# Kernel optimization log

Hardware: AMD Instinct MI355X
Metric: run time of the kernel (lower is better)

The kernel has to match this reference:

```python
import jax, jax.numpy as jnp
import numpy as np

# ---- static config (matches init_kwargs and NSA hyperparams in source) ----
DIM = 512; HEADS = 8; DH = DIM // HEADS; DEPTH = 2
HH = 28; WW = 28; SEQ = HH * WW            # 784
WIN = 28 * 7                                # sliding window = 196
CBS = 28 * 14; CST = 28 * 7                 # compress block 392, stride 196
SBS = 28 * 14; NSEL = 1                     # selection block 392, top-1
NC = (SEQ - CBS) // CST + 1                 # 3 compressed blocks
NS = SEQ // SBS                             # 2 selection blocks
EPS = 1e-5
BATCH = 8


def _overlap_matrix():
    # fraction of each compressed block overlapping each selection block
    O = np.zeros((NC, NS), np.float32)
    for i in range(NC):
        a, b = i * CST, i * CST + CBS
        for j in range(NS):
            c, d = j * SBS, (j + 1) * SBS
            O[i, j] = max(0, min(b, d) - max(a, c)) / CBS
    return jnp.asarray(O)

OVERLAP = _overlap_matrix()  # [NC, NS]


def setup_inputs() -> dict:
    key = jax.random.key(0)
    ks = jax.random.split(key, 12)
    p = lambda i, shape, s=0.02: (jax.random.normal(ks[i], shape, jnp.float32) * s)
    return {
        "x": jax.random.normal(ks[0], (BATCH, DIM, HH, WW), jnp.float32),
        "pos_emb": jax.random.normal(ks[1], (SEQ,), jnp.float32),
        "attn_norm_g": jnp.ones((DEPTH, DIM), jnp.float32),
        "Wq": p(2, (DEPTH, DIM, HEADS * DH)),
        "Wk": p(3, (DEPTH, DIM, HEADS * DH)),
        "Wv": p(4, (DEPTH, DIM, HEADS * DH)),
        "Wo": p(5, (DEPTH, HEADS * DH, DIM)),
        "Wg": p(6, (DEPTH, DIM, HEADS * 3)),
        "ff_norm_g": jnp.ones((DEPTH, DIM), jnp.float32),
        "ff_norm_b": jnp.zeros((DEPTH, DIM), jnp.float32),
        "ff_w1": p(7, (DEPTH, 4 * DIM, DIM)),
        "ff_b1": jnp.zeros((DEPTH, 4 * DIM), jnp.float32),
        "ff_w2": p(8, (DEPTH, DIM, 4 * DIM)),
        "ff_b2": jnp.zeros((DEPTH, DIM), jnp.float32),
    }


def _sparse_attn(x, g, wq, wk, wv, wo, wg):
    # x: [b, n, d]  -- NSA: sliding window + compressed + top-k block selection
    b, n, d = x.shape
    xr = x * jax.lax.rsqrt(jnp.mean(x * x, -1, keepdims=True) + EPS) * g  # RMSNorm
    q = (xr @ wq).reshape(b, n, HEADS, DH)
    k = (xr @ wk).reshape(b, n, HEADS, DH)
    v = (xr @ wv).reshape(b, n, HEADS, DH)
    scale = DH ** -0.5

    # ---- compressed branch: mean-pool overlapping blocks ----
    ck = jnp.stack([k[:, i * CST:i * CST + CBS].mean(1) for i in range(NC)], 1)  # [b,NC,h,dh]
    cv = jnp.stack([v[:, i * CST:i * CST + CBS].mean(1) for i in range(NC)], 1)
    sc = jnp.einsum('bihd,bjhd->bhij', q, ck) * scale          # [b,h,n,NC]
    pc = jax.nn.softmax(sc, -1)
    out_c = jnp.einsum('bhij,bjhd->bihd', pc, cv)              # [b,n,h,dh]

    # ---- selection branch: importance -> top-k selection blocks -> fine attn ----
    imp = jnp.einsum('bhij,jk->bhik', pc, OVERLAP)             # [b,h,n,NS]
    _, sel = jax.lax.top_k(imp, NSEL)                          # [b,h,n,NSEL]
    selmask = jax.nn.one_hot(sel, NS, dtype=jnp.float32).sum(-2) > 0  # [b,h,n,NS]
    blk = jnp.arange(n) // SBS                                 # token -> selection block
    tokmask = selmask[..., blk]                                # [b,h,n,n]
    sf = jnp.einsum('bihd,bjhd->bhij', q, k) * scale           # full fine scores (shared)
    neg = jnp.finfo(sf.dtype).min
    ps = jax.nn.softmax(jnp.where(tokmask, sf, neg), -1)
    out_s = jnp.einsum('bhij,bjhd->bihd', ps, v)

    # ---- sliding window branch ----
    idx = jnp.arange(n)
    winmask = jnp.abs(idx[:, None] - idx[None, :]) < WIN       # [n,n]
    pw = jax.nn.softmax(jnp.where(winmask, sf, neg), -1)
    out_w = jnp.einsum('bhij,bjhd->bihd', pw, v)

    # ---- per-head learned gates over the 3 branches ----
    gates = jax.nn.sigmoid(xr @ wg).reshape(b, n, HEADS, 3)
    o = (gates[..., 0:1] * out_c + gates[..., 1:2] * out_s + gates[..., 2:3] * out_w)
    return o.reshape(b, n, HEADS * DH) @ wo


def _ff(x, g, bb, w1, b1, w2, b2):
    # x: [b,c,h,w]; LayerNorm over channel dim, then 1x1 conv -> GELU -> 1x1 conv
    mean = x.mean(1, keepdims=True)
    var = jnp.var(x, 1, keepdims=True)
    xn = (x - mean) / jnp.sqrt(var + EPS) * g[None, :, None, None] + bb[None, :, None, None]
    h1 = jax.nn.gelu(jnp.einsum('bchw,oc->bohw', xn, w1) + b1[None, :, None, None], approximate=False)
    return jnp.einsum('bchw,oc->bohw', h1, w2) + b2[None, :, None, None]


def reference(x, pos_emb, attn_norm_g, Wq, Wk, Wv, Wo, Wg,
              ff_norm_g, ff_norm_b, ff_w1, ff_b1, ff_w2, ff_b2):
    b, c, h, w = x.shape
    x = x + pos_emb[:h * w].reshape(1, 1, h, w)
    for l in range(DEPTH):
        s = x.reshape(b, c, h * w).transpose(0, 2, 1)          # b (h w) c
        s = _sparse_attn(s, attn_norm_g[l], Wq[l], Wk[l], Wv[l], Wo[l], Wg[l]) + s
        x = s.transpose(0, 2, 1).reshape(b, c, h, w)
        x = _ff(x, ff_norm_g[l], ff_norm_b[l], ff_w1[l], ff_b1[l], ff_w2[l], ff_b2[l]) + x
    return x
```

## Files before the change

kernel.cpp:

```cpp
#include <hip/hip_runtime.h>
#include <hip/hip_bf16.h>
#include <math.h>

#define B_      8
#define DIMC    512
#define SEQ_    784
#define HEADS_  8
#define DH_     64
#define NTOK    (B_*SEQ_)
#define QLD     1560
#define WIN_    196
#define CBS_    392
#define CST_    196
#define NC_     3
#define EPSF    1e-5f
#define FF_     2048
#define TQ_     28
#define MT_     98

typedef __hip_bfloat16 bf16_t;
typedef __attribute__((ext_vector_type(8))) short bf16x8;
typedef __attribute__((ext_vector_type(4))) float floatx4;
typedef __attribute__((ext_vector_type(4))) unsigned int uintx4;
typedef __attribute__((ext_vector_type(2))) unsigned int uintx2;

__device__ __forceinline__ float wsum(float x){
#pragma unroll
  for (int o = 32; o; o >>= 1) x += __shfl_xor(x, o, 64);
  return x;
}
__device__ __forceinline__ float geluf(float x){
  return 0.5f * x * (1.0f + erff(x * 0.70710678118654752f));
}
__device__ __forceinline__ float sigmoidf_(float x){
  return 1.0f / (1.0f + __expf(-x));
}

__global__ __launch_bounds__(256) void k_init(const float* __restrict__ xin,
                                              const float* __restrict__ pos,
                                              float* __restrict__ X){
  __shared__ float tl[32][33];
  int blk = blockIdx.x;
  int ct = blk & 15;
  int pt = (blk >> 4) % 25;
  int b  = blk / (16 * 25);
  int p0 = pt * 32, c0 = ct * 32;
  int tx = threadIdx.x & 31, ty = threadIdx.x >> 5;
#pragma unroll
  for (int i = 0; i < 4; i++){
    int p = p0 + tx;
    if (p < SEQ_) tl[ty + i * 8][tx] = xin[((long)(b * DIMC + c0 + ty + i * 8)) * SEQ_ + p];
  }
  __syncthreads();
#pragma unroll
  for (int i = 0; i < 4; i++){
    int p = p0 + ty + i * 8;
    if (p < SEQ_)
      X[((long)(b * SEQ_ + p)) * DIMC + c0 + tx] = tl[tx][ty + i * 8] + pos[p];
  }
}

__global__ __launch_bounds__(256) void k_final(const float* __restrict__ X,
                                               float* __restrict__ out){
  __shared__ float tl[32][33];
  int blk = blockIdx.x;
  int ct = blk & 15;
  int pt = (blk >> 4) % 25;
  int b  = blk / (16 * 25);
  int p0 = pt * 32, c0 = ct * 32;
  int tx = threadIdx.x & 31, ty = threadIdx.x >> 5;
#pragma unroll
  for (int i = 0; i < 4; i++){
    int p = p0 + ty + i * 8;
    if (p < SEQ_) tl[ty + i * 8][tx] = X[((long)(b * SEQ_ + p)) * DIMC + c0 + tx];
  }
  __syncthreads();
#pragma unroll
  for (int i = 0; i < 4; i++){
    int p = p0 + tx;
    if (p < SEQ_)
      out[((long)(b * DIMC + c0 + ty + i * 8)) * SEQ_ + p] = tl[tx][ty + i * 8];
  }
}

__global__ __launch_bounds__(256) void k_wconv1(const float* __restrict__ Wq,
                                                const float* __restrict__ Wk,
                                                const float* __restrict__ Wv,
                                                const float* __restrict__ Wg,
                                                bf16_t* __restrict__ Wb){
  __shared__ float tl[32][33];
  int blk = blockIdx.x;
  int kt = blk & 15;
  int ntf = (blk >> 4) % 49;
  int l = blk / (16 * 49);
  int n0 = ntf * 32, k0 = kt * 32;
  int tx = threadIdx.x & 31, ty = threadIdx.x >> 5;
#pragma unroll
  for (int i = 0; i < 4; i++){
    int n = n0 + tx, k = k0 + ty + i * 8;
    float v = 0.0f;
    if (n < 1536){
      int which = n >> 9, nn = n & 511;
      const float* W = (which == 0) ? Wq : ((which == 1) ? Wk : Wv);
      v = W[((long)(l * 512 + k)) * 512 + nn];
    } else if (n < QLD){
      v = Wg[((long)(l * 512 + k)) * 24 + (n - 1536)];
    }
    tl[ty + i * 8][tx] = v;
  }
  __syncthreads();
#pragma unroll
  for (int i = 0; i < 4; i++){
    int n = n0 + ty + i * 8, k = k0 + tx;
    if (n < QLD)
      Wb[((long)(l * QLD + n)) * 512 + k] = __float2bfloat16(tl[tx][ty + i * 8]);
  }
}

__global__ __launch_bounds__(256) void k_wconv2(const float* __restrict__ Wo,
                                                bf16_t* __restrict__ Wb){
  __shared__ float tl[32][33];
  int blk = blockIdx.x;
  int kt = blk & 15;
  int ntf = (blk >> 4) & 15;
  int l = blk >> 8;
  int n0 = ntf * 32, k0 = kt * 32;
  int tx = threadIdx.x & 31, ty = threadIdx.x >> 5;
#pragma unroll
  for (int i = 0; i < 4; i++)
    tl[ty + i * 8][tx] = Wo[((long)(l * 512 + k0 + ty + i * 8)) * 512 + n0 + tx];
  __syncthreads();
#pragma unroll
  for (int i = 0; i < 4; i++)
    Wb[((long)(l * 512 + n0 + ty + i * 8)) * 512 + k0 + tx] = __float2bfloat16(tl[tx][ty + i * 8]);
}

__global__ __launch_bounds__(256) void k_cast(const float* __restrict__ src,
                                              bf16_t* __restrict__ dst){
  int idx = blockIdx.x * 256 + threadIdx.x;
  dst[idx] = __float2bfloat16(src[idx]);
}

__global__ __launch_bounds__(256) void k_zero(uintx4* __restrict__ p){
  p[blockIdx.x * 256 + threadIdx.x] = (uintx4){0u, 0u, 0u, 0u};
}

__global__ __launch_bounds__(256) void k_rms(const float* __restrict__ X,
                                             const float* __restrict__ g,
                                             bf16_t* __restrict__ XR){
  int tok = blockIdx.x;
  int tid = threadIdx.x;
  const float* xr = X + (long)tok * DIMC;
  float v0 = xr[tid], v1 = xr[tid + 256];
  float ss = v0 * v0 + v1 * v1;
  ss = wsum(ss);
  __shared__ float red[4];
  if ((tid & 63) == 0) red[tid >> 6] = ss;
  __syncthreads();
  float tot = red[0] + red[1] + red[2] + red[3];
  float r = rsqrtf(tot * (1.0f / DIMC) + EPSF);
  XR[(long)tok * DIMC + tid]       = __float2bfloat16(v0 * r * g[tid]);
  XR[(long)tok * DIMC + tid + 256] = __float2bfloat16(v1 * r * g[tid + 256]);
}

__global__ __launch_bounds__(256) void k_ln(const float* __restrict__ X,
                                            const float* __restrict__ g,
                                            const float* __restrict__ bb,
                                            bf16_t* __restrict__ XN){
  int tok = blockIdx.x;
  int tid = threadIdx.x;
  const float* xr = X + (long)tok * DIMC;
  float v0 = xr[tid], v1 = xr[tid + 256];
  float s = v0 + v1;
  float q = v0 * v0 + v1 * v1;
  s = wsum(s); q = wsum(q);
  __shared__ float r1[4], r2[4];
  if ((tid & 63) == 0){ r1[tid >> 6] = s; r2[tid >> 6] = q; }
  __syncthreads();
  float ts = r1[0] + r1[1] + r1[2] + r1[3];
  float tq = r2[0] + r2[1] + r2[2] + r2[3];
  float mean = ts * (1.0f / DIMC);
  float var  = tq * (1.0f / DIMC) - mean * mean;
  float rinv = rsqrtf(var + EPSF);
  XN[(long)tok * DIMC + tid]       = __float2bfloat16((v0 - mean) * rinv * g[tid]       + bb[tid]);
  XN[(long)tok * DIMC + tid + 256] = __float2bfloat16((v1 - mean) * rinv * g[tid + 256] + bb[tid + 256]);
}

template<int OUTBF, int ACT, int TN, int BK>
__global__ __launch_bounds__(256) void k_mgemm(const bf16_t* __restrict__ A,
                                               const bf16_t* __restrict__ Bm,
                                               float* Cf,
                                               bf16_t* Cb,
                                               const float* __restrict__ bias,
                                               const float* res,
                                               int M, int N, int K, int ldc, int ccol,
                                               bf16_t* VTo){
  constexpr int NTW = TN / 2;
  constexpr int NF  = TN / 32;
  constexpr int KS  = BK / 32;
  constexpr int AVN = (64 * BK) / 2048;
  constexpr int BVN = (TN * BK) / 2048;
  constexpr int RPB = BK / 8;
  constexpr int RST = 256 / RPB;

  int id = blockIdx.x;
  int xcd = id & 7;
  int j = id >> 3;
  int nt = j / 13;
  int mt = xcd * 13 + (j - nt * 13);
  if (mt >= MT_) return;
  int bm = mt * 64, bn = nt * TN;

  __shared__ bf16_t As[2][64][BK + 8];
  __shared__ bf16_t Bs[2][TN][BK + 8];
  int tid = threadIdx.x;
  int w = tid >> 6, lane = tid & 63;
  int wm = (w & 1) * 32, wn = (w >> 1) * NTW;
  int quad = lane >> 4, l16 = lane & 15;

  int vrow = tid / RPB;
  int vcol = (tid % RPB) * 8;
  const bf16_t* ap[AVN];
  const bf16_t* bp[BVN];
#pragma unroll
  for (int i = 0; i < AVN; i++)
    ap[i] = A + (long)(bm + vrow + i * RST) * K + vcol;
#pragma unroll
  for (int i = 0; i < BVN; i++){
    int r = bn + vrow + i * RST;
    if (r >= N) r = N - 1;
    bp[i] = Bm + (long)r * K + vcol;
  }

  floatx4 acc[2][NF];
#pragma unroll
  for (int i = 0; i < 2; i++)
#pragma unroll
    for (int jj = 0; jj < NF; jj++) acc[i][jj] = (floatx4)(0.0f);

  uintx4 aR[AVN], bR[BVN];
#pragma unroll
  for (int i = 0; i < AVN; i++) aR[i] = *(const uintx4*)ap[i];
#pragma unroll
  for (int i = 0; i < BVN; i++) bR[i] = *(const uintx4*)bp[i];

  int nch = K / BK;
  for (int ch = 0; ch < nch; ch++){
    int buf = ch & 1;
#pragma unroll
    for (int i = 0; i < AVN; i++) *(uintx4*)&As[buf][vrow + i * RST][vcol] = aR[i];
#pragma unroll
    for (int i = 0; i < BVN; i++) *(uintx4*)&Bs[buf][vrow + i * RST][vcol] = bR[i];
    __syncthreads();
    if (ch + 1 < nch){
      int ko = (ch + 1) * BK;
#pragma unroll
      for (int i = 0; i < AVN; i++) aR[i] = *(const uintx4*)(ap[i] + ko);
#pragma unroll
      for (int i = 0; i < BVN; i++) bR[i] = *(const uintx4*)(bp[i] + ko);
    }
#pragma unroll
    for (int ks = 0; ks < KS; ks++){
      bf16x8 a0 = *(bf16x8*)&As[buf][wm + l16][ks * 32 + quad * 8];
      bf16x8 a1 = *(bf16x8*)&As[buf][wm + 16 + l16][ks * 32 + quad * 8];
      bf16x8 bf[NF];
#pragma unroll
      for (int f = 0; f < NF; f++)
        bf[f] = *(bf16x8*)&Bs[buf][wn + f * 16 + l16][ks * 32 + quad * 8];
#pragma unroll
      for (int f = 0; f < NF; f++){
        acc[0][f] = __builtin_amdgcn_mfma_f32_16x16x32_bf16(a0, bf[f], acc[0][f], 0, 0, 0);
        acc[1][f] = __builtin_amdgcn_mfma_f32_16x16x32_bf16(a1, bf[f], acc[1][f], 0, 0, 0);
      }
    }
  }
#pragma unroll
  for (int tm = 0; tm < 2; tm++){
#pragma unroll
    for (int tn = 0; tn < NF; tn++){
      int ncol = bn + wn + tn * 16 + l16;
      if (ncol >= N) continue;
#pragma unroll
      for (int reg = 0; reg < 4; reg++){
        long mrow = bm + wm + tm * 16 + quad * 4 + reg;
        float v = acc[tm][tn][reg];
        if (bias) v += bias[ncol];
        if (ACT == 1) v = geluf(v);
        long off = mrow * (long)ldc + ccol + ncol;
        if (res) v += res[off];
        if (OUTBF){
          Cb[off] = __float2bfloat16(v);
          if (VTo && ncol >= 1024 && ncol < 1536){
            int bb2 = (int)(mrow / SEQ_);
            int tok = (int)(mrow - (long)bb2 * SEQ_);
            VTo[((long)(bb2 * 512 + (ncol - 1024))) * 800 + tok] = __float2bfloat16(v);
          }
        }
        else       Cf[off] = v;
      }
    }
  }
}

__global__ __launch_bounds__(512) void k_cpool(const bf16_t* __restrict__ qkvg,
                                               float* __restrict__ ck,
                                               float* __restrict__ cv){
  int bj = blockIdx.x;
  int j = bj % NC_;
  int b = bj / NC_;
  int tid = threadIdx.x;
  int seg = tid & 127;
  int rg  = tid >> 7;
  __shared__ float part[4][1024];
  const bf16_t* base = qkvg + ((long)b * SEQ_ + (long)j * CST_) * QLD + 512;
  float acc[8] = {0.f,0.f,0.f,0.f,0.f,0.f,0.f,0.f};
  for (int r = rg; r < CBS_; r += 4){
    uintx4 v = *(const uintx4*)(base + (long)r * QLD + seg * 8);
    bf16_t tmp[8]; *(uintx4*)tmp = v;
#pragma unroll
    for (int q = 0; q < 8; q++) acc[q] += __bfloat162float(tmp[q]);
  }
#pragma unroll
  for (int q = 0; q < 8; q++) part[rg][seg * 8 + q] = acc[q];
  __syncthreads();
  for (int c = tid; c < 1024; c += 512){
    float s = (part[0][c] + part[1][c]) + (part[2][c] + part[3][c]);
    s *= (1.0f / CBS_);
    if (c < 512) ck[bj * DIMC + c] = s;
    else         cv[bj * DIMC + (c - 512)] = s;
  }
}

__global__ __launch_bounds__(256) void k_attn(const bf16_t* __restrict__ qkvg,
                                              const float* __restrict__ ck,
                                              const float* __restrict__ cv,
                                              const bf16_t* __restrict__ vtg,
                                              bf16_t* __restrict__ oattn){
  int tid = threadIdx.x;
  int w = tid >> 6, lane = tid & 63;
  int quad = lane >> 4, l16 = lane & 15;
  int id = blockIdx.x;
  int xcd = id & 7;
  int j = id >> 3;
  int bh = xcd * 8 + (j / 28);
  int i0 = (j % 28) * TQ_;
  int h = bh & 7, b = bh >> 3;
  const float scale = 0.125f;

  __shared__ bf16_t Qs[32][72];
  __shared__ bf16_t Ks[2][64][72];
  __shared__ bf16_t Wcw[2][32][72];
  __shared__ bf16_t Wcs[2][32][72];
  __shared__ float outc_s[28][64];
  __shared__ int   sel_s[28];
  __shared__ float cw_s[28], cs_s[28], g1_s[28], g2_s[28];
  __shared__ float red_s[4][4][16];

  const long rowBase = (long)b * SEQ_ * QLD + h * 64;

  if (tid < 224){
    int q = tid >> 3, seg = tid & 7;
    uintx4 qv = *(const uintx4*)(qkvg + rowBase + (long)(i0 + q) * QLD + seg * 8);
    *(uintx4*)&Qs[q][seg * 8] = qv;
  } else {
    int u = tid - 224;
    int r = 28 + (u >> 3), seg = u & 7;
    *(uintx4*)&Qs[r][seg * 8] = (uintx4){0u, 0u, 0u, 0u};
  }
  for (int t = tid; t < 2 * 4 * 72; t += 256){
    int bufi = t / (4 * 72);
    int r = 28 + (t / 72) % 4;
    int c = t % 72;
    Wcw[bufi][r][c] = __float2bfloat16(0.0f);
    Wcs[bufi][r][c] = __float2bfloat16(0.0f);
  }
  __syncthreads();

  int r0i = tid >> 3, s0i = tid & 7;
  int r1i = 32 + r0i;
  uintx4 kreg0 = *(const uintx4*)(qkvg + rowBase + (long)r0i * QLD + 512 + s0i * 8);
  uintx4 kreg1 = *(const uintx4*)(qkvg + rowBase + (long)r1i * QLD + 512 + s0i * 8);

  {
    const float* CKp = ck + (long)b * NC_ * DIMC + h * 64 + lane;
    const float* CVp = cv + (long)b * NC_ * DIMC + h * 64 + lane;
    float k0 = CKp[0], k1 = CKp[512], k2 = CKp[1024];
    float v0 = CVp[0], v1 = CVp[512], v2 = CVp[1024];
#pragma unroll
    for (int qp = 0; qp < 7; qp++){
      int qg = w * 7 + qp;
      float qd = __bfloat162float(Qs[qg][lane]);
      float s0 = wsum(qd * k0) * scale;
      float s1 = wsum(qd * k1) * scale;
      float s2 = wsum(qd * k2) * scale;
      float m3 = fmaxf(s0, fmaxf(s1, s2));
      float e0 = __expf(s0 - m3), e1 = __expf(s1 - m3), e2 = __expf(s2 - m3);
      float inv = 1.0f / (e0 + e1 + e2);
      const bf16_t* grow = qkvg + (long)(b * SEQ_ + i0 + qg) * QLD + 1536 + h * 3;
      float g0 = sigmoidf_(__bfloat162float(grow[0]));
      float g1v = sigmoidf_(__bfloat162float(grow[1]));
      float g2v = sigmoidf_(__bfloat162float(grow[2]));
      outc_s[qg][lane] = g0 * (e0 * v0 + e1 * v1 + e2 * v2) * inv;
      int selv = (s2 > s0) ? 1 : 0;
      if (lane == 0){ sel_s[qg] = selv; g1_s[qg] = g1v; g2_s[qg] = g2v; }
    }
  }

  bf16x8 a00 = *(bf16x8*)&Qs[l16][quad * 8];
  bf16x8 a01 = *(bf16x8*)&Qs[l16][32 + quad * 8];
  bf16x8 a10 = *(bf16x8*)&Qs[16 + l16][quad * 8];
  bf16x8 a11 = *(bf16x8*)&Qs[16 + l16][32 + quad * 8];

  __syncthreads();

  int sel0i = sel_s[l16];
  int sel1i = (l16 < 12) ? sel_s[16 + l16] : 0;
  bool sv0 = (sel0i != 0), sv1 = (sel1i != 0);
  int iq0 = i0 + l16, iq1 = i0 + 16 + l16;
  float sw0 = 0.f, ss0 = 0.f, sw1 = 0.f, ss1 = 0.f;

  const bf16_t* vbase = vtg + ((long)(b * 512 + h * 64 + w * 16 + l16)) * 800;
  floatx4 ow0 = (floatx4)(0.0f), ow1 = (floatx4)(0.0f);
  floatx4 os0 = (floatx4)(0.0f), os1 = (floatx4)(0.0f);

  for (int ch = 0; ch < 13; ch++){
    int buf = ch & 1;
    int K0 = ch * 64;
    *(uintx4*)&Ks[buf][r0i][s0i * 8] = kreg0;
    *(uintx4*)&Ks[buf][r1i][s0i * 8] = kreg1;
    __syncthreads();
    if (ch + 1 < 13){
      int c0n = (ch + 1) * 64;
      int t0 = c0n + r0i; if (t0 > 783) t0 = 783;
      int t1 = c0n + r1i; if (t1 > 783) t1 = 783;
      kreg0 = *(const uintx4*)(qkvg + rowBase + (long)t0 * QLD + 512 + s0i * 8);
      kreg1 = *(const uintx4*)(qkvg + rowBase + (long)t1 * QLD + 512 + s0i * 8);
    }
    int tv0 = K0 + quad * 8;      if (tv0 > 792) tv0 = 792;
    int tv1 = K0 + 32 + quad * 8; if (tv1 > 792) tv1 = 792;
    bf16x8 bv0 = *(const bf16x8*)(vbase + tv0);
    bf16x8 bv1 = *(const bf16x8*)(vbase + tv1);
    bf16x8 k0 = *(bf16x8*)&Ks[buf][w * 16 + l16][quad * 8];
    bf16x8 k1 = *(bf16x8*)&Ks[buf][w * 16 + l16][32 + quad * 8];
    floatx4 d0 = (floatx4)(0.0f), d1 = (floatx4)(0.0f);
    d0 = __builtin_amdgcn_mfma_f32_16x16x32_bf16(k0, a00, d0, 0, 0, 0);
    d0 = __builtin_amdgcn_mfma_f32_16x16x32_bf16(k1, a01, d0, 0, 0, 0);
    d1 = __builtin_amdgcn_mfma_f32_16x16x32_bf16(k0, a10, d1, 0, 0, 0);
    d1 = __builtin_amdgcn_mfma_f32_16x16x32_bf16(k1, a11, d1, 0, 0, 0);
    int kb = K0 + w * 16 + quad * 4;
    union { bf16_t hh[4]; uintx2 v; } pw0, ps0, pw1, ps1;
#pragma unroll
    for (int r = 0; r < 4; r++){
      int key = kb + r;
      float ex0 = __expf(d0[r] * scale);
      float ex1 = __expf(d1[r] * scale);
      bool valid = key < 784;
      float vw0 = (valid && key >= iq0 - 195 && key <= iq0 + 195) ? ex0 : 0.0f;
      float vs0 = (valid && ((key >= 392) == sv0))                ? ex0 : 0.0f;
      float vw1 = (valid && key >= iq1 - 195 && key <= iq1 + 195) ? ex1 : 0.0f;
      float vs1 = (valid && ((key >= 392) == sv1))                ? ex1 : 0.0f;
      sw0 += vw0; ss0 += vs0; sw1 += vw1; ss1 += vs1;
      pw0.hh[r] = __float2bfloat16(vw0);
      ps0.hh[r] = __float2bfloat16(vs0);
      pw1.hh[r] = __float2bfloat16(vw1);
      ps1.hh[r] = __float2bfloat16(vs1);
    }
    int kloc = w * 16 + quad * 4;
    *(uintx2*)&Wcw[buf][l16][kloc] = pw0.v;
    *(uintx2*)&Wcs[buf][l16][kloc] = ps0.v;
    if (l16 < 12){
      *(uintx2*)&Wcw[buf][16 + l16][kloc] = pw1.v;
      *(uintx2*)&Wcs[buf][16 + l16][kloc] = ps1.v;
    }
    __syncthreads();
#pragma unroll
    for (int ks = 0; ks < 2; ks++){
      bf16x8 bv = ks ? bv1 : bv0;
      bf16x8 aw0 = *(bf16x8*)&Wcw[buf][l16][ks * 32 + quad * 8];
      bf16x8 aw1 = *(bf16x8*)&Wcw[buf][16 + l16][ks * 32 + quad * 8];
      bf16x8 as0 = *(bf16x8*)&Wcs[buf][l16][ks * 32 + quad * 8];
      bf16x8 as1 = *(bf16x8*)&Wcs[buf][16 + l16][ks * 32 + quad * 8];
      ow0 = __builtin_amdgcn_mfma_f32_16x16x32_bf16(aw0, bv, ow0, 0, 0, 0);
      ow1 = __builtin_amdgcn_mfma_f32_16x16x32_bf16(aw1, bv, ow1, 0, 0, 0);
      os0 = __builtin_amdgcn_mfma_f32_16x16x32_bf16(as0, bv, os0, 0, 0, 0);
      os1 = __builtin_amdgcn_mfma_f32_16x16x32_bf16(as1, bv, os1, 0, 0, 0);
    }
  }

  sw0 += __shfl_xor(sw0, 16, 64); sw0 += __shfl_xor(sw0, 32, 64);
  ss0 += __shfl_xor(ss0, 16, 64); ss0 += __shfl_xor(ss0, 32, 64);
  sw1 += __shfl_xor(sw1, 16, 64); sw1 += __shfl_xor(sw1, 32, 64);
  ss1 += __shfl_xor(ss1, 16, 64); ss1 += __shfl_xor(ss1, 32, 64);
  if (quad == 0){
    red_s[w][0][l16] = sw0; red_s[w][1][l16] = ss0;
    red_s[w][2][l16] = sw1; red_s[w][3][l16] = ss1;
  }
  __syncthreads();
  if (tid < 28){
    int q = tid, t = q >> 4, l = q & 15;
    float sw = 0.f, ss = 0.f;
#pragma unroll
    for (int wv = 0; wv < 4; wv++){ sw += red_s[wv][2 * t][l]; ss += red_s[wv][2 * t + 1][l]; }
    cw_s[q] = g2_s[q] / sw;
    cs_s[q] = g1_s[q] / ss;
  }
  __syncthreads();

  int d = w * 16 + l16;
#pragma unroll
  for (int reg = 0; reg < 4; reg++){
    int q = quad * 4 + reg;
    float o = cw_s[q] * ow0[reg] + cs_s[q] * os0[reg] + outc_s[q][d];
    oattn[((long)(b * SEQ_ + i0 + q)) * DIMC + h * 64 + d] = __float2bfloat16(o);
    int q2 = q + 16;
    if (q2 < 28){
      float o2 = cw_s[q2] * ow1[reg] + cs_s[q2] * os1[reg] + outc_s[q2][d];
      oattn[((long)(b * SEQ_ + i0 + q2)) * DIMC + h * 64 + d] = __float2bfloat16(o2);
    }
  }
}

extern "C" void kernel_launch(void* const* d_in, const int* in_sizes, int n_in,
                              void* d_out, int out_size, void* d_ws, size_t ws_size,
                              hipStream_t stream){
  const float* xin  = (const float*)d_in[0];
  const float* pos  = (const float*)d_in[1];
  const float* angm = (const float*)d_in[2];
  const float* Wq   = (const float*)d_in[3];
  const float* Wk   = (const float*)d_in[4];
  const float* Wv   = (const float*)d_in[5];
  const float* Wo   = (const float*)d_in[6];
  const float* Wg   = (const float*)d_in[7];
  const float* fng  = (const float*)d_in[8];
  const float* fnb  = (const float*)d_in[9];
  const float* fw1  = (const float*)d_in[10];
  const float* fb1  = (const float*)d_in[11];
  const float* fw2  = (const float*)d_in[12];
  const float* fb2  = (const float*)d_in[13];

  char* cw = (char*)d_ws;
  float* X = (float*)cw;             cw += (long)NTOK * 512 * 4;
  bf16_t* XRb = (bf16_t*)cw;         cw += (long)NTOK * 512 * 2;
  bf16_t* OAb = (bf16_t*)cw;         cw += (long)NTOK * 512 * 2;
  bf16_t* SH  = (bf16_t*)cw;         cw += (long)NTOK * FF_ * 2;
  float* CK = (float*)cw;            cw += (long)B_ * NC_ * DIMC * 4;
  float* CV = (float*)cw;            cw += (long)B_ * NC_ * DIMC * 4;
  bf16_t* Wqkvgb = (bf16_t*)cw;      cw += (long)2 * QLD * 512 * 2;
  bf16_t* WOb    = (bf16_t*)cw;      cw += (long)2 * 512 * 512 * 2;
  bf16_t* FW1b   = (bf16_t*)cw;      cw += (long)2 * FF_ * 512 * 2;
  bf16_t* FW2b   = (bf16_t*)cw;      cw += (long)2 * 512 * FF_ * 2;
  bf16_t* VTb    = (bf16_t*)cw;      cw += (long)B_ * 512 * 800 * 2;
  bf16_t* BUFb = SH;
  bf16_t* H1b  = SH;

  k_wconv1<<<2 * 49 * 16, 256, 0, stream>>>(Wq, Wk, Wv, Wg, Wqkvgb);
  k_wconv2<<<2 * 16 * 16, 256, 0, stream>>>(Wo, WOb);
  k_cast<<<(2 * FF_ * 512) / 256, 256, 0, stream>>>(fw1, FW1b);
  k_cast<<<(2 * 512 * FF_) / 256, 256, 0, stream>>>(fw2, FW2b);

  k_zero<<<1600, 256, 0, stream>>>((uintx4*)VTb);

  k_init<<<8 * 25 * 16, 256, 0, stream>>>(xin, pos, X);

  for (int l = 0; l < 2; l++){
    k_rms<<<NTOK, 256, 0, stream>>>(X, angm + (long)l * DIMC, XRb);

    k_mgemm<1, 0, 128, 32><<<13 * 104, 256, 0, stream>>>(
        XRb, Wqkvgb + (long)l * QLD * 512, nullptr, BUFb, nullptr, nullptr,
        NTOK, QLD, 512, QLD, 0, VTb);

    k_cpool<<<B_ * NC_, 512, 0, stream>>>(BUFb, CK, CV);

    k_attn<<<8 * 8 * 28, 256, 0, stream>>>(BUFb, CK, CV, VTb, OAb);

    k_mgemm<0, 0, 64, 64><<<8 * 104, 256, 0, stream>>>(
        OAb, WOb + (long)l * 512 * 512, X, nullptr, nullptr, X,
        NTOK, 512, 512, 512, 0, nullptr);

    k_ln<<<NTOK, 256, 0, stream>>>(X, fng + (long)l * DIMC, fnb + (long)l * DIMC, XRb);

    k_mgemm<1, 1, 128, 32><<<16 * 104, 256, 0, stream>>>(
        XRb, FW1b + (long)l * FF_ * 512, nullptr, H1b, fb1 + (long)l * FF_, nullptr,
        NTOK, FF_, 512, FF_, 0, nullptr);
    k_mgemm<0, 0, 64, 64><<<8 * 104, 256, 0, stream>>>(
        H1b, FW2b + (long)l * 512 * FF_, X, nullptr, fb2 + (long)l * DIMC, X,
        NTOK, 512, FF_, 512, 0, nullptr);
  }

  k_final<<<8 * 25 * 16, 256, 0, stream>>>(X, (float*)d_out);
}
```

Measured before the change: 575.3 us.

## Widen attention block to 512 threads with 128-key chunks and split-K reduction

The attention kernel now runs 8 waves per block and processes 128 keys per chunk (7 chunks instead of 13). The two wave halves each handle 64 keys of the P·V product and combine partial accumulators through shared memory at the end. The double-buffered K/P tiles become single-buffered, the exp is rewritten as exp2 with a folded scale, and the window and selection masks are precomputed as integer bounds. This roughly halves the chunk-loop iterations and synchronisations per block, at the cost of an extra cross-wave reduction and more shared memory per block.

```diff
diff --git a/kernel.cpp b/kernel.cpp
--- a/kernel.cpp
+++ b/kernel.cpp
@@ -331,7 +331,7 @@
   }
 }
 
-__global__ __launch_bounds__(256) void k_attn(const bf16_t* __restrict__ qkvg,
+__global__ __launch_bounds__(512) void k_attn(const bf16_t* __restrict__ qkvg,
                                               const float* __restrict__ ck,
                                               const float* __restrict__ cv,
                                               const bf16_t* __restrict__ vtg,
@@ -345,16 +345,16 @@
   int bh = xcd * 8 + (j / 28);
   int i0 = (j % 28) * TQ_;
   int h = bh & 7, b = bh >> 3;
-  const float scale = 0.125f;
+  const float SCL2 = 0.18033688011112042f;
 
   __shared__ bf16_t Qs[32][72];
-  __shared__ bf16_t Ks[2][64][72];
-  __shared__ bf16_t Wcw[2][32][72];
-  __shared__ bf16_t Wcs[2][32][72];
+  __shared__ bf16_t Ks[128][72];
+  __shared__ bf16_t Wcw[32][136];
+  __shared__ bf16_t Wcs[32][136];
   __shared__ float outc_s[28][64];
   __shared__ int   sel_s[28];
   __shared__ float cw_s[28], cs_s[28], g1_s[28], g2_s[28];
-  __shared__ float red_s[4][4][16];
+  __shared__ float red_s[8][4][16];
 
   const long rowBase = (long)b * SEQ_ * QLD + h * 64;
 
@@ -362,22 +362,15 @@
     int q = tid >> 3, seg = tid & 7;
     uintx4 qv = *(const uintx4*)(qkvg + rowBase + (long)(i0 + q) * QLD + seg * 8);
     *(uintx4*)&Qs[q][seg * 8] = qv;
-  } else {
+  } else if (tid < 256){
     int u = tid - 224;
     int r = 28 + (u >> 3), seg = u & 7;
     *(uintx4*)&Qs[r][seg * 8] = (uintx4){0u, 0u, 0u, 0u};
   }
-  for (int t = tid; t < 2 * 4 * 72; t += 256){
-    int bufi = t / (4 * 72);
-    int r = 28 + (t / 72) % 4;
-    int c = t % 72;
-    Wcw[bufi][r][c] = __float2bfloat16(0.0f);
-    Wcs[bufi][r][c] = __float2bfloat16(0.0f);
-  }
   __syncthreads();
 
   int r0i = tid >> 3, s0i = tid & 7;
-  int r1i = 32 + r0i;
+  int r1i = 64 + r0i;
   uintx4 kreg0 = *(const uintx4*)(qkvg + rowBase + (long)r0i * QLD + 512 + s0i * 8);
   uintx4 kreg1 = *(const uintx4*)(qkvg + rowBase + (long)r1i * QLD + 512 + s0i * 8);
 
@@ -387,12 +380,13 @@
     float k0 = CKp[0], k1 = CKp[512], k2 = CKp[1024];
     float v0 = CVp[0], v1 = CVp[512], v2 = CVp[1024];
 #pragma unroll
-    for (int qp = 0; qp < 7; qp++){
-      int qg = w * 7 + qp;
+    for (int qp = 0; qp < 4; qp++){
+      int qg = w * 4 + qp;
+      if (qg >= 28) break;
       float qd = __bfloat162float(Qs[qg][lane]);
-      float s0 = wsum(qd * k0) * scale;
-      float s1 = wsum(qd * k1) * scale;
-      float s2 = wsum(qd * k2) * scale;
+      float s0 = wsum(qd * k0) * 0.125f;
+      float s1 = wsum(qd * k1) * 0.125f;
+      float s2 = wsum(qd * k2) * 0.125f;
       float m3 = fmaxf(s0, fmaxf(s1, s2));
       float e0 = __expf(s0 - m3), e1 = __expf(s1 - m3), e2 = __expf(s2 - m3);
       float inv = 1.0f / (e0 + e1 + e2);
@@ -413,35 +407,37 @@
 
   __syncthreads();
 
-  int sel0i = sel_s[l16];
-  int sel1i = (l16 < 12) ? sel_s[16 + l16] : 0;
-  bool sv0 = (sel0i != 0), sv1 = (sel1i != 0);
   int iq0 = i0 + l16, iq1 = i0 + 16 + l16;
+  int sv0 = sel_s[l16];
+  int sv1 = (l16 < 12) ? sel_s[16 + l16] : 0;
+  int wlo0 = iq0 - 195, whi0 = (iq0 + 195 > 783) ? 783 : iq0 + 195;
+  int wlo1 = iq1 - 195, whi1 = (iq1 + 195 > 783) ? 783 : iq1 + 195;
+  int slo0 = sv0 ? 392 : 0, shi0 = sv0 ? 783 : 391;
+  int slo1 = sv1 ? 392 : 0, shi1 = sv1 ? 783 : 391;
   float sw0 = 0.f, ss0 = 0.f, sw1 = 0.f, ss1 = 0.f;
 
-  const bf16_t* vbase = vtg + ((long)(b * 512 + h * 64 + w * 16 + l16)) * 800;
+  int kh = (w >> 2) * 64;
+  const bf16_t* vbase = vtg + ((long)(b * 512 + h * 64 + (w & 3) * 16 + l16)) * 800;
   floatx4 ow0 = (floatx4)(0.0f), ow1 = (floatx4)(0.0f);
   floatx4 os0 = (floatx4)(0.0f), os1 = (floatx4)(0.0f);
 
-  for (int ch = 0; ch < 13; ch++){
-    int buf = ch & 1;
-    int K0 = ch * 64;
-    *(uintx4*)&Ks[buf][r0i][s0i * 8] = kreg0;
-    *(uintx4*)&Ks[buf][r1i][s0i * 8] = kreg1;
+  for (int ch = 0; ch < 7; ch++){
+    int K0 = ch * 128;
+    *(uintx4*)&Ks[r0i][s0i * 8] = kreg0;
+    *(uintx4*)&Ks[r1i][s0i * 8] = kreg1;
     __syncthreads();
-    if (ch + 1 < 13){
-      int c0n = (ch + 1) * 64;
-      int t0 = c0n + r0i; if (t0 > 783) t0 = 783;
-      int t1 = c0n + r1i; if (t1 > 783) t1 = 783;
+    if (ch + 1 < 7){
+      int t0 = K0 + 128 + r0i; if (t0 > 783) t0 = 783;
+      int t1 = K0 + 128 + r1i; if (t1 > 783) t1 = 783;
       kreg0 = *(const uintx4*)(qkvg + rowBase + (long)t0 * QLD + 512 + s0i * 8);
       kreg1 = *(const uintx4*)(qkvg + rowBase + (long)t1 * QLD + 512 + s0i * 8);
     }
-    int tv0 = K0 + quad * 8;      if (tv0 > 792) tv0 = 792;
-    int tv1 = K0 + 32 + quad * 8; if (tv1 > 792) tv1 = 792;
+    int tv0 = K0 + kh + quad * 8;      if (tv0 > 792) tv0 = 792;
+    int tv1 = K0 + kh + 32 + quad * 8; if (tv1 > 792) tv1 = 792;
     bf16x8 bv0 = *(const bf16x8*)(vbase + tv0);
     bf16x8 bv1 = *(const bf16x8*)(vbase + tv1);
-    bf16x8 k0 = *(bf16x8*)&Ks[buf][w * 16 + l16][quad * 8];
-    bf16x8 k1 = *(bf16x8*)&Ks[buf][w * 16 + l16][32 + quad * 8];
+    bf16x8 k0 = *(bf16x8*)&Ks[w * 16 + l16][quad * 8];
+    bf16x8 k1 = *(bf16x8*)&Ks[w * 16 + l16][32 + quad * 8];
     floatx4 d0 = (floatx4)(0.0f), d1 = (floatx4)(0.0f);
     d0 = __builtin_amdgcn_mfma_f32_16x16x32_bf16(k0, a00, d0, 0, 0, 0);
     d0 = __builtin_amdgcn_mfma_f32_16x16x32_bf16(k1, a01, d0, 0, 0, 0);
@@ -452,13 +448,12 @@
 #pragma unroll
     for (int r = 0; r < 4; r++){
       int key = kb + r;
-      float ex0 = __expf(d0[r] * scale);
-      float ex1 = __expf(d1[r] * scale);
-      bool valid = key < 784;
-      float vw0 = (valid && key >= iq0 - 195 && key <= iq0 + 195) ? ex0 : 0.0f;
-      float vs0 = (valid && ((key >= 392) == sv0))                ? ex0 : 0.0f;
-      float vw1 = (valid && key >= iq1 - 195 && key <= iq1 + 195) ? ex1 : 0.0f;
-      float vs1 = (valid && ((key >= 392) == sv1))                ? ex1 : 0.0f;
+      float ex0 = exp2f(d0[r] * SCL2);
+      float ex1 = exp2f(d1[r] * SCL2);
+      float vw0 = (key >= wlo0 && key <= whi0) ? ex0 : 0.0f;
+      float vs0 = (key >= slo0 && key <= shi0) ? ex0 : 0.0f;
+      float vw1 = (key >= wlo1 && key <= whi1) ? ex1 : 0.0f;
+      float vs1 = (key >= slo1 && key <= shi1) ? ex1 : 0.0f;
       sw0 += vw0; ss0 += vs0; sw1 += vw1; ss1 += vs1;
       pw0.hh[r] = __float2bfloat16(vw0);
       ps0.hh[r] = __float2bfloat16(vs0);
@@ -466,20 +461,21 @@
       ps1.hh[r] = __float2bfloat16(vs1);
     }
     int kloc = w * 16 + quad * 4;
-    *(uintx2*)&Wcw[buf][l16][kloc] = pw0.v;
-    *(uintx2*)&Wcs[buf][l16][kloc] = ps0.v;
+    *(uintx2*)&Wcw[l16][kloc] = pw0.v;
+    *(uintx2*)&Wcs[l16][kloc] = ps0.v;
     if (l16 < 12){
-      *(uintx2*)&Wcw[buf][16 + l16][kloc] = pw1.v;
-      *(uintx2*)&Wcs[buf][16 + l16][kloc] = ps1.v;
+      *(uintx2*)&Wcw[16 + l16][kloc] = pw1.v;
+      *(uintx2*)&Wcs[16 + l16][kloc] = ps1.v;
     }
     __syncthreads();
 #pragma unroll
     for (int ks = 0; ks < 2; ks++){
       bf16x8 bv = ks ? bv1 : bv0;
-      bf16x8 aw0 = *(bf16x8*)&Wcw[buf][l16][ks * 32 + quad * 8];
-      bf16x8 aw1 = *(bf16x8*)&Wcw[buf][16 + l16][ks * 32 + quad * 8];
-      bf16x8 as0 = *(bf16x8*)&Wcs[buf][l16][ks * 32 + quad * 8];
-      bf16x8 as1 = *(bf16x8*)&Wcs[buf][16 + l16][ks * 32 + quad * 8];
+      int kc = kh + ks * 32 + quad * 8;
+      bf16x8 aw0 = *(bf16x8*)&Wcw[l16][kc];
+      bf16x8 aw1 = *(bf16x8*)&Wcw[16 + l16][kc];
+      bf16x8 as0 = *(bf16x8*)&Wcs[l16][kc];
+      bf16x8 as1 = *(bf16x8*)&Wcs[16 + l16][kc];
       ow0 = __builtin_amdgcn_mfma_f32_16x16x32_bf16(aw0, bv, ow0, 0, 0, 0);
       ow1 = __builtin_amdgcn_mfma_f32_16x16x32_bf16(aw1, bv, ow1, 0, 0, 0);
       os0 = __builtin_amdgcn_mfma_f32_16x16x32_bf16(as0, bv, os0, 0, 0, 0);
@@ -495,27 +491,44 @@
     red_s[w][0][l16] = sw0; red_s[w][1][l16] = ss0;
     red_s[w][2][l16] = sw1; red_s[w][3][l16] = ss1;
   }
+  float* red = (float*)&Ks[0][0];
+  if (w >= 4){
+    int base = ((w - 4) * 64 + lane) * 16;
+    *(floatx4*)&red[base + 0]  = ow0;
+    *(floatx4*)&red[base + 4]  = ow1;
+    *(floatx4*)&red[base + 8]  = os0;
+    *(floatx4*)&red[base + 12] = os1;
+  }
   __syncthreads();
   if (tid < 28){
     int q = tid, t = q >> 4, l = q & 15;
     float sw = 0.f, ss = 0.f;
 #pragma unroll
-    for (int wv = 0; wv < 4; wv++){ sw += red_s[wv][2 * t][l]; ss += red_s[wv][2 * t + 1][l]; }
+    for (int wv = 0; wv < 8; wv++){ sw += red_s[wv][2 * t][l]; ss += red_s[wv][2 * t + 1][l]; }
     cw_s[q] = g2_s[q] / sw;
     cs_s[q] = g1_s[q] / ss;
   }
-  __syncthreads();
-
-  int d = w * 16 + l16;
-#pragma unroll
-  for (int reg = 0; reg < 4; reg++){
-    int q = quad * 4 + reg;
-    float o = cw_s[q] * ow0[reg] + cs_s[q] * os0[reg] + outc_s[q][d];
-    oattn[((long)(b * SEQ_ + i0 + q)) * DIMC + h * 64 + d] = __float2bfloat16(o);
-    int q2 = q + 16;
-    if (q2 < 28){
-      float o2 = cw_s[q2] * ow1[reg] + cs_s[q2] * os1[reg] + outc_s[q2][d];
-      oattn[((long)(b * SEQ_ + i0 + q2)) * DIMC + h * 64 + d] = __float2bfloat16(o2);
+  if (w < 4){
+    int base = (w * 64 + lane) * 16;
+    ow0 += *(floatx4*)&red[base + 0];
+    ow1 += *(floatx4*)&red[base + 4];
+    os0 += *(floatx4*)&red[base + 8];
+    os1 += *(floatx4*)&red[base + 12];
+  }
+  __syncthreads();
+
+  if (w < 4){
+    int d = w * 16 + l16;
+#pragma unroll
+    for (int reg = 0; reg < 4; reg++){
+      int q = quad * 4 + reg;
+      float o = cw_s[q] * ow0[reg] + cs_s[q] * os0[reg] + outc_s[q][d];
+      oattn[((long)(b * SEQ_ + i0 + q)) * DIMC + h * 64 + d] = __float2bfloat16(o);
+      int q2 = q + 16;
+      if (q2 < 28){
+        float o2 = cw_s[q2] * ow1[reg] + cs_s[q2] * os1[reg] + outc_s[q2][d];
+        oattn[((long)(b * SEQ_ + i0 + q2)) * DIMC + h * 64 + d] = __float2bfloat16(o2);
+      }
     }
   }
 }
@@ -571,7 +584,7 @@
 
     k_cpool<<<B_ * NC_, 512, 0, stream>>>(BUFb, CK, CV);
 
-    k_attn<<<8 * 8 * 28, 256, 0, stream>>>(BUFb, CK, CV, VTb, OAb);
+    k_attn<<<8 * 8 * 28, 512, 0, stream>>>(BUFb, CK, CV, VTb, OAb);
 
     k_mgemm<0, 0, 64, 64><<<8 * 104, 256, 0, stream>>>(
         OAb, WOb + (long)l * 512 * 512, X, nullptr, nullptr, X,
```

Measured after the change: 595.2 us. 1.03x slower.

## Stage GEMM tiles via direct global-to-LDS loads with double buffering

Applied to the files above, without the earlier changes.

Replaces the register-staged global loads and LDS stores in the MFMA GEMM with global_load_lds 16-byte direct transfers, split across the four waves. The main loop is restructured into an unrolled ping-pong over two LDS buffers, with the next chunk issued before the current one is computed. LDS padding is removed, which can introduce bank conflicts on the MFMA operand reads. The loop assumes an even number of K chunks, and it relies on the builtin's implicit lane-to-address mapping, which must line up with the LDS layout.

```diff
diff --git a/kernel.cpp b/kernel.cpp
--- a/kernel.cpp
+++ b/kernel.cpp
@@ -35,6 +35,11 @@
 __device__ __forceinline__ float sigmoidf_(float x){
   return 1.0f / (1.0f + __expf(-x));
 }
+__device__ __forceinline__ void gload16(const bf16_t* g, bf16_t* l){
+  __builtin_amdgcn_global_load_lds(
+      (const __attribute__((address_space(1))) void*)g,
+      (__attribute__((address_space(3))) void*)l, 16, 0, 0);
+}
 
 __global__ __launch_bounds__(256) void k_init(const float* __restrict__ xin,
                                               const float* __restrict__ pos,
@@ -195,13 +200,16 @@
                                                const float* res,
                                                int M, int N, int K, int ldc, int ccol,
                                                bf16_t* VTo){
-  constexpr int NTW = TN / 2;
-  constexpr int NF  = TN / 32;
-  constexpr int KS  = BK / 32;
-  constexpr int AVN = (64 * BK) / 2048;
-  constexpr int BVN = (TN * BK) / 2048;
-  constexpr int RPB = BK / 8;
-  constexpr int RST = 256 / RPB;
+  constexpr int NTW  = TN / 2;
+  constexpr int NF   = TN / 32;
+  constexpr int KS   = BK / 32;
+  constexpr int RPB2 = 512 / BK;
+  constexpr int LPR  = BK / 8;
+  constexpr int ABLK = BK / 8;
+  constexpr int BBLK = (TN * BK) / 512;
+  constexpr int TOT  = ABLK + BBLK;
+  constexpr int PW   = TOT / 4;
+  static_assert(TOT % 4 == 0, "stage blocks must split across 4 waves");
 
   int id = blockIdx.x;
   int xcd = id & 7;
@@ -211,25 +219,31 @@
   if (mt >= MT_) return;
   int bm = mt * 64, bn = nt * TN;
 
-  __shared__ bf16_t As[2][64][BK + 8];
-  __shared__ bf16_t Bs[2][TN][BK + 8];
+  __shared__ bf16_t As[2][64][BK];
+  __shared__ bf16_t Bs[2][TN][BK];
   int tid = threadIdx.x;
   int w = tid >> 6, lane = tid & 63;
   int wm = (w & 1) * 32, wn = (w >> 1) * NTW;
   int quad = lane >> 4, l16 = lane & 15;
 
-  int vrow = tid / RPB;
-  int vcol = (tid % RPB) * 8;
-  const bf16_t* ap[AVN];
-  const bf16_t* bp[BVN];
-#pragma unroll
-  for (int i = 0; i < AVN; i++)
-    ap[i] = A + (long)(bm + vrow + i * RST) * K + vcol;
-#pragma unroll
-  for (int i = 0; i < BVN; i++){
-    int r = bn + vrow + i * RST;
-    if (r >= N) r = N - 1;
-    bp[i] = Bm + (long)r * K + vcol;
+  int lr = lane / LPR, lc = (lane % LPR) * 8;
+  const bf16_t* gsrc[PW];
+  bf16_t* ldst0[PW];
+  bf16_t* ldst1[PW];
+#pragma unroll
+  for (int i = 0; i < PW; i++){
+    int bi = w * PW + i;
+    if (bi < ABLK){
+      gsrc[i]  = A + (long)(bm + bi * RPB2 + lr) * K + lc;
+      ldst0[i] = &As[0][bi * RPB2][0];
+      ldst1[i] = &As[1][bi * RPB2][0];
+    } else {
+      int bj = bi - ABLK;
+      int r = bn + bj * RPB2 + lr; if (r >= N) r = N - 1;
+      gsrc[i]  = Bm + (long)r * K + lc;
+      ldst0[i] = &Bs[0][bj * RPB2][0];
+      ldst1[i] = &Bs[1][bj * RPB2][0];
+    }
   }
 
   floatx4 acc[2][NF];
@@ -238,42 +252,40 @@
 #pragma unroll
     for (int jj = 0; jj < NF; jj++) acc[i][jj] = (floatx4)(0.0f);
 
-  uintx4 aR[AVN], bR[BVN];
-#pragma unroll
-  for (int i = 0; i < AVN; i++) aR[i] = *(const uintx4*)ap[i];
-#pragma unroll
-  for (int i = 0; i < BVN; i++) bR[i] = *(const uintx4*)bp[i];
+#define MG_STAGE0(ko) do { _Pragma("unroll") \
+    for (int i_ = 0; i_ < PW; i_++) gload16(gsrc[i_] + (ko), ldst0[i_]); } while (0)
+#define MG_STAGE1(ko) do { _Pragma("unroll") \
+    for (int i_ = 0; i_ < PW; i_++) gload16(gsrc[i_] + (ko), ldst1[i_]); } while (0)
+#define MG_COMPUTE(BUFI) do { _Pragma("unroll") \
+    for (int ks_ = 0; ks_ < KS; ks_++){ \
+      bf16x8 a0_ = *(bf16x8*)&As[BUFI][wm + l16][ks_ * 32 + quad * 8]; \
+      bf16x8 a1_ = *(bf16x8*)&As[BUFI][wm + 16 + l16][ks_ * 32 + quad * 8]; \
+      bf16x8 bf_[NF]; \
+      _Pragma("unroll") \
+      for (int f_ = 0; f_ < NF; f_++) \
+        bf_[f_] = *(bf16x8*)&Bs[BUFI][wn + f_ * 16 + l16][ks_ * 32 + quad * 8]; \
+      _Pragma("unroll") \
+      for (int f_ = 0; f_ < NF; f_++){ \
+        acc[0][f_] = __builtin_amdgcn_mfma_f32_16x16x32_bf16(a0_, bf_[f_], acc[0][f_], 0, 0, 0); \
+        acc[1][f_] = __builtin_amdgcn_mfma_f32_16x16x32_bf16(a1_, bf_[f_], acc[1][f_], 0, 0, 0); \
+      } \
+    } } while (0)
 
   int nch = K / BK;
-  for (int ch = 0; ch < nch; ch++){
-    int buf = ch & 1;
-#pragma unroll
-    for (int i = 0; i < AVN; i++) *(uintx4*)&As[buf][vrow + i * RST][vcol] = aR[i];
-#pragma unroll
-    for (int i = 0; i < BVN; i++) *(uintx4*)&Bs[buf][vrow + i * RST][vcol] = bR[i];
+  MG_STAGE0(0);
+  __syncthreads();
+  for (int ch = 0; ch < nch; ch += 2){
+    MG_STAGE1((ch + 1) * BK);
+    MG_COMPUTE(0);
     __syncthreads();
-    if (ch + 1 < nch){
-      int ko = (ch + 1) * BK;
-#pragma unroll
-      for (int i = 0; i < AVN; i++) aR[i] = *(const uintx4*)(ap[i] + ko);
-#pragma unroll
-      for (int i = 0; i < BVN; i++) bR[i] = *(const uintx4*)(bp[i] + ko);
-    }
-#pragma unroll
-    for (int ks = 0; ks < KS; ks++){
-      bf16x8 a0 = *(bf16x8*)&As[buf][wm + l16][ks * 32 + quad * 8];
-      bf16x8 a1 = *(bf16x8*)&As[buf][wm + 16 + l16][ks * 32 + quad * 8];
-      bf16x8 bf[NF];
-#pragma unroll
-      for (int f = 0; f < NF; f++)
-        bf[f] = *(bf16x8*)&Bs[buf][wn + f * 16 + l16][ks * 32 + quad * 8];
-#pragma unroll
-      for (int f = 0; f < NF; f++){
-        acc[0][f] = __builtin_amdgcn_mfma_f32_16x16x32_bf16(a0, bf[f], acc[0][f], 0, 0, 0);
-        acc[1][f] = __builtin_amdgcn_mfma_f32_16x16x32_bf16(a1, bf[f], acc[1][f], 0, 0, 0);
-      }
-    }
-  }
+    if (ch + 2 < nch) MG_STAGE0((ch + 2) * BK);
+    MG_COMPUTE(1);
+    __syncthreads();
+  }
+#undef MG_STAGE0
+#undef MG_STAGE1
+#undef MG_COMPUTE
+
 #pragma unroll
   for (int tm = 0; tm < 2; tm++){
 #pragma unroll
```

Result: no change. 577.7 us (+0.4%).
